# Optimization experiments

Hardware: AMD Instinct MI355X
Metric: run time of the kernel (lower is better)

Reference implementation:

```python
import math
import jax, jax.numpy as jnp
import numpy as np

B, C_IN, C_OUT, K, STYLE, H, W = 16, 512, 512, 3, 512, 64, 64


def setup_inputs() -> dict:
    key = jax.random.key(0)
    k1, k2, k3, k4 = jax.random.split(key, 4)
    return {
        "x": jax.random.normal(k1, (B, C_IN, H, W), jnp.float32),
        "style": jax.random.normal(k2, (B, STYLE), jnp.float32),
        "weight": jax.random.normal(k3, (C_OUT, C_IN, K, K), jnp.float32),  # learned conv weight (leading 1 dim of torch param squeezed)
        "mod_w": jax.random.normal(k4, (C_IN, STYLE), jnp.float32),         # EqualLinear weight
        "mod_b": jnp.ones((C_IN,), jnp.float32),                             # EqualLinear bias (bias_init=1)
    }


def reference(x, style, weight, mod_w, mod_b):
    # EqualLinear modulation: scale = 1/sqrt(style_dim), lr_mul = 1
    mod_scale = 1.0 / math.sqrt(STYLE)
    s = style @ (mod_w.T * mod_scale) + mod_b            # [B, C_IN]

    # per-sample modulated weight
    w_scale = 1.0 / math.sqrt(C_IN * K * K)
    w = w_scale * weight[None] * s[:, None, :, None, None]  # [B, C_OUT, C_IN, K, K]

    # demodulate
    demod = jax.lax.rsqrt(jnp.sum(w * w, axis=(2, 3, 4)) + 1e-8)  # [B, C_OUT]
    w = w * demod[:, :, None, None, None]

    pad = K // 2

    def conv_one(xi, wi):
        # xi: [C_IN, H, W], wi: [C_OUT, C_IN, K, K]
        return jax.lax.conv_general_dilated(
            xi[None], wi, window_strides=(1, 1),
            padding=[(pad, pad), (pad, pad)],
            dimension_numbers=("NCHW", "OIHW", "NCHW"),
        )[0]

    return jax.vmap(conv_one)(x, w)  # [B, C_OUT, H, W]
```

## Files before the change

### kernel.cpp

```cpp
#include <hip/hip_runtime.h>
#include <hip/hip_bf16.h>
#include <math.h>
#include <stdint.h>

#define B_     16
#define CI_    512
#define CO_    512
#define HH     64
#define WW     64
#define STYLE_ 512

typedef __bf16 bf16x8 __attribute__((ext_vector_type(8)));
typedef float f32x16 __attribute__((ext_vector_type(16)));

__device__ __forceinline__ int fsl(int r, int h) {
    return (2 * r + (h ^ ((r >> 2) & 1))) ^ (((r >> 4) & 1) << 1);
}

#define WS_S     0
#define WS_DEMOD 32768
#define WS_WSQ   65536
#define WS_WB    1114112
#define WS_XS    5832704

__device__ __forceinline__ void gload16(const void* g, void* l) {
    __builtin_amdgcn_global_load_lds((const __attribute__((address_space(1))) uint32_t*)g,
                                     (__attribute__((address_space(3))) uint32_t*)l, 16, 0, 0);
}

__global__ __launch_bounds__(256) void k_style2(const float* __restrict__ style,
                                                const float* __restrict__ mod_w,
                                                const float* __restrict__ mod_b,
                                                float* __restrict__ s_out) {
    const int ci   = blockIdx.x * 4 + (threadIdx.x >> 6);
    const int b    = blockIdx.y;
    const int lane = threadIdx.x & 63;
    const float4* mw = (const float4*)(mod_w + (size_t)ci * STYLE_);
    const float4* st = (const float4*)(style + (size_t)b * STYLE_);
    float acc = 0.f;
    #pragma unroll
    for (int i = 0; i < 2; ++i) {
        float4 a = mw[lane + i * 64], s = st[lane + i * 64];
        acc += a.x * s.x + a.y * s.y + a.z * s.z + a.w * s.w;
    }
    #pragma unroll
    for (int off = 32; off >= 1; off >>= 1) acc += __shfl_xor(acc, off);
    if (lane == 0)
        s_out[b * CI_ + ci] = acc * 0.044194173824159216f + mod_b[ci];
}

__global__ __launch_bounds__(256) void k_wprep(const float* __restrict__ weight,
                                               float* __restrict__ wsq, __bf16* __restrict__ wb) {
    int p = blockIdx.x * 256 + threadIdx.x;
    int co = p >> 9, ci = p & 511;
    const float* wp = weight + (size_t)p * 9;
    const int gs = ((co >> 6) << 7) + fsl(co & 63, (ci >> 3) & 1);
    float acc = 0.f;
    #pragma unroll
    for (int t = 0; t < 9; ++t) {
        float v = wp[t];
        acc += v * v;
        wb[(((size_t)(ci >> 4) * 9 + t) * 8192) + gs * 8 + (ci & 7)] = (__bf16)v;
    }
    wsq[(size_t)ci * CO_ + co] = acc;
}

__global__ void k_demod(const float* __restrict__ s, const float* __restrict__ wsq,
                        float* __restrict__ demod) {
    int b = blockIdx.x, co = threadIdx.x;
    const float w_scale2 = 1.0f / 4608.0f;
    float acc = 0.f;
    const float* sb = s + b * CI_;
    for (int ci = 0; ci < CI_; ++ci) { float sv = sb[ci]; acc += sv * sv * wsq[(size_t)ci * CO_ + co]; }
    demod[b * CO_ + co] = 1.0f / sqrtf(acc * w_scale2 + 1e-8f);
}

__global__ __launch_bounds__(256) void k_xs(const float* __restrict__ x, const float* __restrict__ s,
                                            __bf16* __restrict__ xs) {
    __shared__ float Lt[64][65];
    const int y = blockIdx.x, b = blockIdx.y;
    const int tid = threadIdx.x;
    const float w_scale = 0.014731391274719739f;
    for (int ci0 = 0; ci0 < CI_; ci0 += 64) {
        for (int i = tid; i < 64 * 16; i += 256) {
            int ci = i >> 4, x4 = (i & 15) * 4;
            const float4 v = *(const float4*)&x[((size_t)(b * CI_ + ci0 + ci) * HH + y) * WW + x4];
            float sc = s[b * CI_ + ci0 + ci] * w_scale;
            Lt[ci][x4]     = v.x * sc;
            Lt[ci][x4 + 1] = v.y * sc;
            Lt[ci][x4 + 2] = v.z * sc;
            Lt[ci][x4 + 3] = v.w * sc;
        }
        __syncthreads();
        for (int o = tid; o < 512; o += 256) {
            int xx = o >> 3, oct = o & 7;
            int cb = ci0 + oct * 8;
            int chunk = cb >> 4;
            int pp = fsl(xx + 1, oct & 1) - 2;
            bf16x8 v;
            #pragma unroll
            for (int j = 0; j < 8; ++j) v[j] = (__bf16)Lt[oct * 8 + j][xx];
            size_t idx = (((size_t)chunk * 16 + b) * 66 + (y + 1)) * 1024 + pp * 8;
            *(bf16x8*)&xs[idx] = v;
        }
        __syncthreads();
    }
    if (y == 0 || y == 63) {
        const int row = (y == 0) ? 0 : 65;
        uint32_t* xs32 = (uint32_t*)xs;
        for (int c = 0; c < 32; ++c)
            for (int i = tid; i < 512; i += 256)
                xs32[(((size_t)c * 16 + b) * 66 + row) * 512 + i] = 0;
    }
}

#define XBUF 21120
#define WBUF 18432

__global__ __launch_bounds__(256, 2) void k_conv(
    const __bf16* __restrict__ xs, const __bf16* __restrict__ wb,
    const float* __restrict__ demod, float* __restrict__ out)
{
    __shared__ __align__(128) char smem[2 * XBUF + 2 * WBUF];

    const int tid  = threadIdx.x;
    const int lane = tid & 63;
    const int wave = tid >> 6;

    const int bid  = blockIdx.x;
    const int r8   = bid & 7;
    const int q    = bid >> 3;
    const int co0  = (q & 7) * 64;
    const int tt   = q >> 3;
    const int y0   = (tt & 7) * 8;
    const int b    = r8 * 2 + (tt >> 3);

    const int lm = lane & 31;
    const int g2 = lane >> 5;

    for (int i = tid; i < 320; i += 256) {
        int buf = i / 160, rem = i % 160;
        int rb = rem >> 4, hh = rem & 15;
        int side = hh >> 3, dw = hh & 7;
        ((uint32_t*)smem)[buf * (XBUF / 4) + rb * 528 + side * 520 + dw] = 0;
    }
    asm volatile("s_waitcnt lgkmcnt(0)" ::: "memory");

    uint32_t soff[10];
    uint32_t sdst[10];
    if (wave < 2) {
        #pragma unroll
        for (int i = 0; i < 10; ++i) {
            int j = wave * 10 + i, rb = j >> 1, seg = j & 1;
            soff[i] = (uint32_t)((y0 + rb) * 1024 + seg * 512 + lane * 8);
            sdst[i] = (uint32_t)(rb * 2112 + 32 + seg * 1024 + lane * 16);
        }
    } else {
        #pragma unroll
        for (int i = 0; i < 9; ++i) {
            int j = (wave - 2) * 9 + i;
            int tap = j >> 1, seg = j & 1;
            soff[i] = (uint32_t)(tap * 8192 + co0 * 16 + seg * 512 + lane * 8);
            sdst[i] = (uint32_t)(j * 1024 + lane * 16);
        }
        soff[9] = 0; sdst[9] = 0;
    }

    const uint32_t acol = (uint32_t)(16 * fsl(lm, g2));
    uint32_t cbase[3];
    #pragma unroll
    for (int kw = 0; kw < 3; ++kw) cbase[kw] = (uint32_t)(16 * fsl(lm + kw, g2));
    uint32_t rbase[4];
    #pragma unroll
    for (int rr = 0; rr < 4; ++rr) rbase[rr] = (uint32_t)((2 * wave + rr) * 2112);

    f32x16 acc[2][4];
    #pragma unroll
    for (int mi = 0; mi < 2; ++mi)
        #pragma unroll
        for (int n = 0; n < 4; ++n)
            #pragma unroll
            for (int r = 0; r < 16; ++r) acc[mi][n][r] = 0.f;

    auto stage = [&](int chunk, int sel) {
        if (wave < 2) {
            const __bf16* base = xs + (size_t)chunk * 1081344 + (size_t)b * 67584;
            #pragma unroll
            for (int i = 0; i < 10; ++i) gload16(base + soff[i], smem + sel * XBUF + sdst[i]);
        } else {
            const __bf16* base = wb + (size_t)chunk * 73728;
            #pragma unroll
            for (int i = 0; i < 9; ++i) gload16(base + soff[i], smem + 2 * XBUF + sel * WBUF + sdst[i]);
        }
    };

    stage(0, 0);

    for (int t = 0; t < 32; ++t) {
        if (t < 31) {
            stage(t + 1, (t + 1) & 1);
            if (wave < 2) asm volatile("s_waitcnt vmcnt(10)" ::: "memory");
            else          asm volatile("s_waitcnt vmcnt(9)"  ::: "memory");
        } else {
            asm volatile("s_waitcnt vmcnt(0)" ::: "memory");
        }
        __builtin_amdgcn_s_barrier();

        const char* xbuf = smem + (t & 1) * XBUF;
        const char* wbuf = smem + 2 * XBUF + (t & 1) * WBUF + acol;

        __builtin_amdgcn_s_setprio(1);
        #pragma unroll
        for (int kw = 0; kw < 3; ++kw) {
            bf16x8 fa[3][2], fb[4][2];
            #pragma unroll
            for (int kh = 0; kh < 3; ++kh) {
                const char* wp = wbuf + (kh * 3 + kw) * 2048;
                fa[kh][0] = *(const bf16x8*)(wp);
                fa[kh][1] = *(const bf16x8*)(wp + 1024);
            }
            #pragma unroll
            for (int rr = 0; rr < 4; ++rr) {
                fb[rr][0] = *(const bf16x8*)(xbuf + rbase[rr] + cbase[kw]);
                fb[rr][1] = *(const bf16x8*)(xbuf + rbase[rr] + cbase[kw] + 1024);
            }
            #pragma unroll
            for (int kh = 0; kh < 3; ++kh)
                #pragma unroll
                for (int ys = 0; ys < 2; ++ys)
                    #pragma unroll
                    for (int nt = 0; nt < 2; ++nt) {
                        acc[0][ys * 2 + nt] = __builtin_amdgcn_mfma_f32_32x32x16_bf16(
                            fa[kh][0], fb[ys + kh][nt], acc[0][ys * 2 + nt], 0, 0, 0);
                        acc[1][ys * 2 + nt] = __builtin_amdgcn_mfma_f32_32x32x16_bf16(
                            fa[kh][1], fb[ys + kh][nt], acc[1][ys * 2 + nt], 0, 0, 0);
                    }
        }
        __builtin_amdgcn_s_setprio(0);
        __builtin_amdgcn_s_barrier();
    }

    #pragma unroll
    for (int mi = 0; mi < 2; ++mi) {
        #pragma unroll
        for (int ys = 0; ys < 2; ++ys) {
            const int y = y0 + 2 * wave + ys;
            float* outb = out + ((size_t)b * CO_ + co0 + mi * 32) * 4096 + (size_t)y * 64;
            #pragma unroll
            for (int reg = 0; reg < 16; ++reg) {
                const int cosub = (reg & 3) + 8 * (reg >> 2) + 4 * g2;
                const float dm = demod[b * CO_ + co0 + mi * 32 + cosub];
                outb[(size_t)cosub * 4096 + lm]      = acc[mi][ys * 2 + 0][reg] * dm;
                outb[(size_t)cosub * 4096 + 32 + lm] = acc[mi][ys * 2 + 1][reg] * dm;
            }
        }
    }
}

extern "C" void kernel_launch(void* const* d_in, const int* in_sizes, int n_in,
                              void* d_out, int out_size, void* d_ws, size_t ws_size,
                              hipStream_t stream) {
    const float* x      = (const float*)d_in[0];
    const float* style  = (const float*)d_in[1];
    const float* weight = (const float*)d_in[2];
    const float* mod_w  = (const float*)d_in[3];
    const float* mod_b  = (const float*)d_in[4];
    float* out = (float*)d_out;

    char* wsb = (char*)d_ws;
    float*  s_buf = (float*)(wsb + WS_S);
    float*  demod = (float*)(wsb + WS_DEMOD);
    float*  wsq   = (float*)(wsb + WS_WSQ);
    __bf16* wb    = (__bf16*)(wsb + WS_WB);
    __bf16* xs    = (__bf16*)(wsb + WS_XS);

    k_style2<<<dim3(CI_ / 4, B_), dim3(256), 0, stream>>>(style, mod_w, mod_b, s_buf);
    k_wprep<<<dim3(CO_ * CI_ / 256), dim3(256), 0, stream>>>(weight, wsq, wb);
    k_demod<<<dim3(B_), dim3(CO_), 0, stream>>>(s_buf, wsq, demod);
    k_xs<<<dim3(HH, B_), dim3(256), 0, stream>>>(x, s_buf, xs);
    k_conv<<<dim3(1024), dim3(256), 0, stream>>>(xs, wb, demod, out);
}
```

Measured before the change: 319.7 us.

## Split demod across more blocks, reorder xs writes, and stagger wave priorities in conv

```diff
diff --git a/kernel.cpp b/kernel.cpp
--- a/kernel.cpp
+++ b/kernel.cpp
@@ -65,12 +65,14 @@
     wsq[(size_t)ci * CO_ + co] = acc;
 }
 
-__global__ void k_demod(const float* __restrict__ s, const float* __restrict__ wsq,
-                        float* __restrict__ demod) {
-    int b = blockIdx.x, co = threadIdx.x;
+__global__ __launch_bounds__(64) void k_demod(const float* __restrict__ s,
+                                              const float* __restrict__ wsq,
+                                              float* __restrict__ demod) {
+    int b = blockIdx.x, co = blockIdx.y * 64 + threadIdx.x;
     const float w_scale2 = 1.0f / 4608.0f;
     float acc = 0.f;
     const float* sb = s + b * CI_;
+    #pragma unroll 8
     for (int ci = 0; ci < CI_; ++ci) { float sv = sb[ci]; acc += sv * sv * wsq[(size_t)ci * CO_ + co]; }
     demod[b * CO_ + co] = 1.0f / sqrtf(acc * w_scale2 + 1e-8f);
 }
@@ -92,8 +94,10 @@
             Lt[ci][x4 + 3] = v.w * sc;
         }
         __syncthreads();
-        for (int o = tid; o < 512; o += 256) {
-            int xx = o >> 3, oct = o & 7;
+        #pragma unroll
+        for (int it = 0; it < 2; ++it) {
+            int o = tid + it * 256;
+            int xx = o & 63, oct = o >> 6;
             int cb = ci0 + oct * 8;
             int chunk = cb >> 4;
             int pp = fsl(xx + 1, oct & 1) - 2;
@@ -134,6 +138,7 @@
     const int tt   = q >> 3;
     const int y0   = (tt & 7) * 8;
     const int b    = r8 * 2 + (tt >> 3);
+    const int pbit = (bid ^ (bid >> 8) ^ (bid >> 9)) & 1;
 
     const int lm = lane & 31;
     const int g2 = lane >> 5;
@@ -196,49 +201,53 @@
 
     stage(0, 0);
 
-    for (int t = 0; t < 32; ++t) {
-        if (t < 31) {
-            stage(t + 1, (t + 1) & 1);
-            if (wave < 2) asm volatile("s_waitcnt vmcnt(10)" ::: "memory");
-            else          asm volatile("s_waitcnt vmcnt(9)"  ::: "memory");
-        } else {
-            asm volatile("s_waitcnt vmcnt(0)" ::: "memory");
-        }
-        __builtin_amdgcn_s_barrier();
-
-        const char* xbuf = smem + (t & 1) * XBUF;
-        const char* wbuf = smem + 2 * XBUF + (t & 1) * WBUF + acol;
-
-        __builtin_amdgcn_s_setprio(1);
-        #pragma unroll
-        for (int kw = 0; kw < 3; ++kw) {
-            bf16x8 fa[3][2], fb[4][2];
-            #pragma unroll
-            for (int kh = 0; kh < 3; ++kh) {
-                const char* wp = wbuf + (kh * 3 + kw) * 2048;
-                fa[kh][0] = *(const bf16x8*)(wp);
-                fa[kh][1] = *(const bf16x8*)(wp + 1024);
-            }
-            #pragma unroll
-            for (int rr = 0; rr < 4; ++rr) {
-                fb[rr][0] = *(const bf16x8*)(xbuf + rbase[rr] + cbase[kw]);
-                fb[rr][1] = *(const bf16x8*)(xbuf + rbase[rr] + cbase[kw] + 1024);
-            }
-            #pragma unroll
-            for (int kh = 0; kh < 3; ++kh)
-                #pragma unroll
-                for (int ys = 0; ys < 2; ++ys)
-                    #pragma unroll
-                    for (int nt = 0; nt < 2; ++nt) {
-                        acc[0][ys * 2 + nt] = __builtin_amdgcn_mfma_f32_32x32x16_bf16(
-                            fa[kh][0], fb[ys + kh][nt], acc[0][ys * 2 + nt], 0, 0, 0);
-                        acc[1][ys * 2 + nt] = __builtin_amdgcn_mfma_f32_32x32x16_bf16(
-                            fa[kh][1], fb[ys + kh][nt], acc[1][ys * 2 + nt], 0, 0, 0);
-                    }
-        }
-        __builtin_amdgcn_s_setprio(0);
-        __builtin_amdgcn_s_barrier();
-    }
+#define MAIN_LOOP(PHI, PLO)                                                        \
+    for (int t = 0; t < 32; ++t) {                                                 \
+        if (t < 31) {                                                              \
+            stage(t + 1, (t + 1) & 1);                                             \
+            if (wave < 2) asm volatile("s_waitcnt vmcnt(10)" ::: "memory");        \
+            else          asm volatile("s_waitcnt vmcnt(9)"  ::: "memory");        \
+        } else {                                                                   \
+            asm volatile("s_waitcnt vmcnt(0)" ::: "memory");                       \
+        }                                                                          \
+        __builtin_amdgcn_s_barrier();                                              \
+        const char* xbuf = smem + (t & 1) * XBUF;                                  \
+        const char* wbuf = smem + 2 * XBUF + (t & 1) * WBUF + acol;                \
+        _Pragma("unroll")                                                          \
+        for (int kw = 0; kw < 3; ++kw) {                                           \
+            bf16x8 fa[3][2], fb[4][2];                                             \
+            _Pragma("unroll")                                                      \
+            for (int kh = 0; kh < 3; ++kh) {                                       \
+                const char* wp = wbuf + (kh * 3 + kw) * 2048;                      \
+                fa[kh][0] = *(const bf16x8*)(wp);                                  \
+                fa[kh][1] = *(const bf16x8*)(wp + 1024);                           \
+            }                                                                      \
+            _Pragma("unroll")                                                      \
+            for (int rr = 0; rr < 4; ++rr) {                                       \
+                fb[rr][0] = *(const bf16x8*)(xbuf + rbase[rr] + cbase[kw]);        \
+                fb[rr][1] = *(const bf16x8*)(xbuf + rbase[rr] + cbase[kw] + 1024); \
+            }                                                                      \
+            __builtin_amdgcn_s_setprio(PHI);                                       \
+            _Pragma("unroll")                                                      \
+            for (int kh = 0; kh < 3; ++kh)                                         \
+                _Pragma("unroll")                                                  \
+                for (int ys = 0; ys < 2; ++ys)                                     \
+                    _Pragma("unroll")                                              \
+                    for (int nt = 0; nt < 2; ++nt) {                               \
+                        acc[0][ys * 2 + nt] = __builtin_amdgcn_mfma_f32_32x32x16_bf16( \
+                            fa[kh][0], fb[ys + kh][nt], acc[0][ys * 2 + nt], 0, 0, 0); \
+                        acc[1][ys * 2 + nt] = __builtin_amdgcn_mfma_f32_32x32x16_bf16( \
+                            fa[kh][1], fb[ys + kh][nt], acc[1][ys * 2 + nt], 0, 0, 0); \
+                    }                                                              \
+            __builtin_amdgcn_s_setprio(PLO);                                       \
+        }                                                                          \
+        __builtin_amdgcn_s_barrier();                                              \
+    }
+
+    if (pbit) { __builtin_amdgcn_s_setprio(2); MAIN_LOOP(3, 2) }
+    else      {                                MAIN_LOOP(1, 0) }
+    __builtin_amdgcn_s_setprio(0);
+#undef MAIN_LOOP
 
     #pragma unroll
     for (int mi = 0; mi < 2; ++mi) {
@@ -276,7 +285,7 @@
 
     k_style2<<<dim3(CI_ / 4, B_), dim3(256), 0, stream>>>(style, mod_w, mod_b, s_buf);
     k_wprep<<<dim3(CO_ * CI_ / 256), dim3(256), 0, stream>>>(weight, wsq, wb);
-    k_demod<<<dim3(B_), dim3(CO_), 0, stream>>>(s_buf, wsq, demod);
+    k_demod<<<dim3(B_, CO_ / 64), dim3(64), 0, stream>>>(s_buf, wsq, demod);
     k_xs<<<dim3(HH, B_), dim3(256), 0, stream>>>(x, s_buf, xs);
     k_conv<<<dim3(1024), dim3(256), 0, stream>>>(xs, wb, demod, out);
 }
```

New measurement: 332.2 us. +3.9%, slower.
